# Kernel optimization log

Hardware: AMD Instinct MI355X
Metric: run time of the kernel (lower is better)

## Reference

```python
import jax, jax.numpy as jnp
import numpy as np
from itertools import permutations

EPS = 1e-14


def setup_inputs() -> dict:
    key = jax.random.key(0)
    k1, k2 = jax.random.split(key)
    B, T, S = 512, 8000, 3
    pred = jax.random.normal(k1, (B, T, S), dtype=jnp.float32)
    targets = (jax.random.uniform(k2, (B, T, S)) < 0.3).astype(jnp.float32)
    mask = jnp.ones((B, T), dtype=jnp.float32)
    return {"pred_frames_out": pred, "targets": targets, "mask": mask}


def _pit_loss(pred, targets, mask):
    # pred, targets: [B, T, S]; mask: [B, T]
    B, T, S = pred.shape
    x = pred[:, :, :, None]        # [B,T,S_pred,1]
    t = targets[:, :, None, :]     # [B,T,1,S_tgt]
    # numerically stable BCE-with-logits (same as nn.BCEWithLogitsLoss)
    bce = jnp.maximum(x, 0.0) - x * t + jnp.log1p(jnp.exp(-jnp.abs(x)))  # [B,T,S,S]
    msum = jnp.sum(mask, axis=1) + EPS                                    # [B]
    # cost[b,i,j] = masked mean over time of BCE(pred_i, target_j)
    cost = jnp.einsum('btij,bt->bij', bce, mask) / msum[:, None, None]    # [B,S,S]
    perms = jnp.asarray(list(permutations(range(S))), dtype=jnp.int32)    # [P,S]
    idx_i = jnp.arange(S)[None, :]                                        # [1,S]
    # perm_loss[b,p] = mean_i cost[b, i, perms[p,i]]
    perm_loss = jnp.mean(cost[:, idx_i, perms], axis=-1)                  # [B,P]
    best_val = jnp.min(perm_loss, axis=1)                                 # [B]
    best_idx = jnp.argmin(perm_loss, axis=1)                              # [B]
    return best_val.mean(), best_idx


def reference(pred_frames_out, targets, mask):
    return _pit_loss(pred_frames_out, targets, mask)
```

## Files before the change

kernel.cpp:

```cpp
#include <hip/hip_runtime.h>
#include <math.h>

#define BB 512
#define TT 8000
#define CH 4
#define TC (TT/CH)
#define NACC 13

__device__ __forceinline__ void accum_elem(float acc[NACC], float m,
                                           float x0, float x1, float x2,
                                           float t0, float t1, float t2) {
    acc[12] += m;
    float x[3] = {x0, x1, x2};
    float t[3] = {t0, t1, t2};
    #pragma unroll
    for (int i = 0; i < 3; i++) {
        float xi = x[i];
        float sp = fmaxf(xi, 0.0f) + __logf(1.0f + __expf(-fabsf(xi)));
        acc[i] = fmaf(m, sp, acc[i]);
        float mx = m * xi;
        #pragma unroll
        for (int j = 0; j < 3; j++)
            acc[3 + i*3 + j] = fmaf(mx, t[j], acc[3 + i*3 + j]);
    }
}

__global__ __launch_bounds__(256) void pit_partial(
        const float* __restrict__ pred,
        const float* __restrict__ tgt,
        const float* __restrict__ mask,
        float* __restrict__ bpart) {
    __shared__ float red[4][16];

    int blk = blockIdx.x;
    int b = blk >> 2, c = blk & 3;
    const float* pp = pred + ((size_t)b * TT + c * TC) * 3;
    const float* tp = tgt  + ((size_t)b * TT + c * TC) * 3;
    const float* mp = mask + (size_t)b * TT + c * TC;

    int tid = threadIdx.x;
    float acc[NACC];
    #pragma unroll
    for (int k = 0; k < NACC; k++) acc[k] = 0.0f;

    #pragma unroll
    for (int it = 0; it < 8; it++) {
        int t = tid + it * 256;
        int tc_ = t < TC ? t : TC - 1;
        float3 x3 = *(const float3*)(pp + 3 * (size_t)tc_);
        float3 g3 = *(const float3*)(tp + 3 * (size_t)tc_);
        float m = mp[tc_];
        m = (t < TC) ? m : 0.0f;
        accum_elem(acc, m, x3.x, x3.y, x3.z, g3.x, g3.y, g3.z);
    }

    #pragma unroll
    for (int k = 0; k < NACC; k++) {
        float v = acc[k];
        #pragma unroll
        for (int o = 32; o > 0; o >>= 1) v += __shfl_xor(v, o, 64);
        acc[k] = v;
    }

    int lane = tid & 63, w = tid >> 6;
    if (lane == 0) {
        #pragma unroll
        for (int k = 0; k < NACC; k++) red[w][k] = acc[k];
        red[w][13] = 0.0f; red[w][14] = 0.0f; red[w][15] = 0.0f;
    }
    __syncthreads();
    if (tid < 16) {
        float s = red[0][tid] + red[1][tid] + red[2][tid] + red[3][tid];
        bpart[(size_t)blk * 16 + tid] = s;
    }
}

__global__ __launch_bounds__(512) void pit_final(
        const float* __restrict__ bpart, float* __restrict__ out) {
    __shared__ double sd[8];
    int b = threadIdx.x;

    double a[NACC];
    #pragma unroll
    for (int k = 0; k < NACC; k++) a[k] = 0.0;
    const float* r = bpart + (size_t)b * 64;
    #pragma unroll
    for (int c = 0; c < CH; c++)
        #pragma unroll
        for (int k = 0; k < NACC; k++)
            a[k] += (double)r[c * 16 + k];

    double msum = a[12] + 1e-14;
    double cost[3][3];
    #pragma unroll
    for (int i = 0; i < 3; i++)
        #pragma unroll
        for (int j = 0; j < 3; j++)
            cost[i][j] = (a[i] - a[3 + i*3 + j]) / msum;

    const int perms[6][3] = {{0,1,2},{0,2,1},{1,0,2},{1,2,0},{2,0,1},{2,1,0}};
    double best = 1e300; int bidx = 0;
    #pragma unroll
    for (int p = 0; p < 6; p++) {
        double v = (cost[0][perms[p][0]] + cost[1][perms[p][1]] +
                    cost[2][perms[p][2]]) / 3.0;
        if (v < best) { best = v; bidx = p; }
    }
    out[1 + b] = (float)bidx;

    double v = best;
    #pragma unroll
    for (int o = 32; o > 0; o >>= 1) v += __shfl_down(v, o, 64);
    int lane = b & 63, w = b >> 6;
    if (lane == 0) sd[w] = v;
    __syncthreads();
    if (b == 0) {
        double s = 0.0;
        #pragma unroll
        for (int i = 0; i < 8; i++) s += sd[i];
        out[0] = (float)(s / (double)BB);
    }
}

extern "C" void kernel_launch(void* const* d_in, const int* in_sizes, int n_in,
                              void* d_out, int out_size, void* d_ws, size_t ws_size,
                              hipStream_t stream) {
    const float* pred = (const float*)d_in[0];
    const float* tgt  = (const float*)d_in[1];
    const float* mask = (const float*)d_in[2];
    float* out = (float*)d_out;
    float* bpart = (float*)d_ws;

    pit_partial<<<BB * CH, 256, 0, stream>>>(pred, tgt, mask, bpart);
    pit_final<<<1, 512, 0, stream>>>(bpart, out);
}
```

Measured before the change: 30.30 us.

## Use one 1024-thread block per batch and compute the permutation cost in-block

Replaces 4 blocks of 256 threads per batch with a single 1024-thread block per batch. The cost matrix and best permutation are now computed inside each block, so the final kernel only averages 512 doubles. This moves the per-batch double-precision work out of the serial single-block kernel and shrinks the workspace. The trade-offs are fewer, larger blocks (512), which may hurt occupancy and load balance across CUs, and a serial 16-way shared-memory sum done by one thread.

```diff
diff --git a/kernel.cpp b/kernel.cpp
--- a/kernel.cpp
+++ b/kernel.cpp
@@ -3,9 +3,8 @@
 
 #define BB 512
 #define TT 8000
-#define CH 4
-#define TC (TT/CH)
 #define NACC 13
+#define NW 16
 
 __device__ __forceinline__ void accum_elem(float acc[NACC], float m,
                                            float x0, float x1, float x2,
@@ -25,18 +24,18 @@
     }
 }
 
-__global__ __launch_bounds__(256) void pit_partial(
+__global__ __launch_bounds__(1024) void pit_batch(
         const float* __restrict__ pred,
         const float* __restrict__ tgt,
         const float* __restrict__ mask,
-        float* __restrict__ bpart) {
-    __shared__ float red[4][16];
+        double* __restrict__ bestv,
+        float* __restrict__ out) {
+    __shared__ float red[NW][16];
 
-    int blk = blockIdx.x;
-    int b = blk >> 2, c = blk & 3;
-    const float* pp = pred + ((size_t)b * TT + c * TC) * 3;
-    const float* tp = tgt  + ((size_t)b * TT + c * TC) * 3;
-    const float* mp = mask + (size_t)b * TT + c * TC;
+    int b = blockIdx.x;
+    const float* pp = pred + (size_t)b * TT * 3;
+    const float* tp = tgt  + (size_t)b * TT * 3;
+    const float* mp = mask + (size_t)b * TT;
 
     int tid = threadIdx.x;
     float acc[NACC];
@@ -45,12 +44,12 @@
 
     #pragma unroll
     for (int it = 0; it < 8; it++) {
-        int t = tid + it * 256;
-        int tc_ = t < TC ? t : TC - 1;
+        int t = tid + it * 1024;
+        int tc_ = t < TT ? t : TT - 1;
         float3 x3 = *(const float3*)(pp + 3 * (size_t)tc_);
         float3 g3 = *(const float3*)(tp + 3 * (size_t)tc_);
         float m = mp[tc_];
-        m = (t < TC) ? m : 0.0f;
+        m = (t < TT) ? m : 0.0f;
         accum_elem(acc, m, x3.x, x3.y, x3.z, g3.x, g3.y, g3.z);
     }
 
@@ -66,49 +65,45 @@
     if (lane == 0) {
         #pragma unroll
         for (int k = 0; k < NACC; k++) red[w][k] = acc[k];
-        red[w][13] = 0.0f; red[w][14] = 0.0f; red[w][15] = 0.0f;
     }
     __syncthreads();
-    if (tid < 16) {
-        float s = red[0][tid] + red[1][tid] + red[2][tid] + red[3][tid];
-        bpart[(size_t)blk * 16 + tid] = s;
+
+    if (tid == 0) {
+        double a[NACC];
+        #pragma unroll
+        for (int k = 0; k < NACC; k++) {
+            double s = 0.0;
+            #pragma unroll
+            for (int i = 0; i < NW; i++) s += (double)red[i][k];
+            a[k] = s;
+        }
+        double msum = a[12] + 1e-14;
+        double cost[3][3];
+        #pragma unroll
+        for (int i = 0; i < 3; i++)
+            #pragma unroll
+            for (int j = 0; j < 3; j++)
+                cost[i][j] = (a[i] - a[3 + i*3 + j]) / msum;
+
+        const int perms[6][3] = {{0,1,2},{0,2,1},{1,0,2},
+                                 {1,2,0},{2,0,1},{2,1,0}};
+        double best = 1e300; int bidx = 0;
+        #pragma unroll
+        for (int p = 0; p < 6; p++) {
+            double v = (cost[0][perms[p][0]] + cost[1][perms[p][1]] +
+                        cost[2][perms[p][2]]) / 3.0;
+            if (v < best) { best = v; bidx = p; }
+        }
+        bestv[b] = best;
+        out[1 + b] = (float)bidx;
     }
 }
 
-__global__ __launch_bounds__(512) void pit_final(
-        const float* __restrict__ bpart, float* __restrict__ out) {
+__global__ __launch_bounds__(512) void pit_mean(
+        const double* __restrict__ bestv, float* __restrict__ out) {
     __shared__ double sd[8];
     int b = threadIdx.x;
-
-    double a[NACC];
-    #pragma unroll
-    for (int k = 0; k < NACC; k++) a[k] = 0.0;
-    const float* r = bpart + (size_t)b * 64;
-    #pragma unroll
-    for (int c = 0; c < CH; c++)
-        #pragma unroll
-        for (int k = 0; k < NACC; k++)
-            a[k] += (double)r[c * 16 + k];
-
-    double msum = a[12] + 1e-14;
-    double cost[3][3];
-    #pragma unroll
-    for (int i = 0; i < 3; i++)
-        #pragma unroll
-        for (int j = 0; j < 3; j++)
-            cost[i][j] = (a[i] - a[3 + i*3 + j]) / msum;
-
-    const int perms[6][3] = {{0,1,2},{0,2,1},{1,0,2},{1,2,0},{2,0,1},{2,1,0}};
-    double best = 1e300; int bidx = 0;
-    #pragma unroll
-    for (int p = 0; p < 6; p++) {
-        double v = (cost[0][perms[p][0]] + cost[1][perms[p][1]] +
-                    cost[2][perms[p][2]]) / 3.0;
-        if (v < best) { best = v; bidx = p; }
-    }
-    out[1 + b] = (float)bidx;
-
-    double v = best;
+    double v = bestv[b];
     #pragma unroll
     for (int o = 32; o > 0; o >>= 1) v += __shfl_down(v, o, 64);
     int lane = b & 63, w = b >> 6;
@@ -129,8 +124,8 @@
     const float* tgt  = (const float*)d_in[1];
     const float* mask = (const float*)d_in[2];
     float* out = (float*)d_out;
-    float* bpart = (float*)d_ws;
+    double* bestv = (double*)d_ws;
 
-    pit_partial<<<BB * CH, 256, 0, stream>>>(pred, tgt, mask, bpart);
-    pit_final<<<1, 512, 0, stream>>>(bpart, out);
+    pit_batch<<<BB, 1024, 0, stream>>>(pred, tgt, mask, bestv, out);
+    pit_mean<<<1, 512, 0, stream>>>(bestv, out);
 }
```

Result: slower. 35.24 us (+16.3%).

## Halve block count per batch and batch loads four-deep per thread

Applied to the files above, without the earlier changes.

Each batch row is now split into two chunks of 4000 frames instead of four chunks of 2000, so 1024 blocks each process 16 frames per thread. Loads are grouped four at a time before the compute step, which exposes more memory-level parallelism per thread. The final kernel sums two partials per batch instead of four. This trades fewer blocks and less partial-sum traffic for longer per-thread loops and fewer waves available to hide latency on the device.

```diff
diff --git a/kernel.cpp b/kernel.cpp
--- a/kernel.cpp
+++ b/kernel.cpp
@@ -3,8 +3,7 @@
 
 #define BB 512
 #define TT 8000
-#define CH 4
-#define TC (TT/CH)
+#define HALF 4000
 #define NACC 13
 
 __device__ __forceinline__ void accum_elem(float acc[NACC], float m,
@@ -33,10 +32,11 @@
     __shared__ float red[4][16];
 
     int blk = blockIdx.x;
-    int b = blk >> 2, c = blk & 3;
-    const float* pp = pred + ((size_t)b * TT + c * TC) * 3;
-    const float* tp = tgt  + ((size_t)b * TT + c * TC) * 3;
-    const float* mp = mask + (size_t)b * TT + c * TC;
+    int b = blk >> 1, h = blk & 1;
+    int base = h * HALF;
+    const float* pp = pred + (size_t)b * TT * 3;
+    const float* tp = tgt  + (size_t)b * TT * 3;
+    const float* mp = mask + (size_t)b * TT;
 
     int tid = threadIdx.x;
     float acc[NACC];
@@ -44,14 +44,22 @@
     for (int k = 0; k < NACC; k++) acc[k] = 0.0f;
 
     #pragma unroll
-    for (int it = 0; it < 8; it++) {
-        int t = tid + it * 256;
-        int tc_ = t < TC ? t : TC - 1;
-        float3 x3 = *(const float3*)(pp + 3 * (size_t)tc_);
-        float3 g3 = *(const float3*)(tp + 3 * (size_t)tc_);
-        float m = mp[tc_];
-        m = (t < TC) ? m : 0.0f;
-        accum_elem(acc, m, x3.x, x3.y, x3.z, g3.x, g3.y, g3.z);
+    for (int g = 0; g < 4; g++) {
+        float3 X[4], G[4]; float M[4];
+        #pragma unroll
+        for (int u = 0; u < 4; u++) {
+            int t = base + tid + (g * 4 + u) * 256;
+            int hi = base + HALF;
+            int tc_ = t < hi ? t : hi - 1;
+            X[u] = *(const float3*)(pp + 3 * (size_t)tc_);
+            G[u] = *(const float3*)(tp + 3 * (size_t)tc_);
+            float m = mp[tc_];
+            M[u] = (t < hi) ? m : 0.0f;
+        }
+        #pragma unroll
+        for (int u = 0; u < 4; u++)
+            accum_elem(acc, M[u], X[u].x, X[u].y, X[u].z,
+                       G[u].x, G[u].y, G[u].z);
     }
 
     #pragma unroll
@@ -81,14 +89,10 @@
     int b = threadIdx.x;
 
     double a[NACC];
+    const float* r = bpart + (size_t)b * 32;
     #pragma unroll
-    for (int k = 0; k < NACC; k++) a[k] = 0.0;
-    const float* r = bpart + (size_t)b * 64;
-    #pragma unroll
-    for (int c = 0; c < CH; c++)
-        #pragma unroll
-        for (int k = 0; k < NACC; k++)
-            a[k] += (double)r[c * 16 + k];
+    for (int k = 0; k < NACC; k++)
+        a[k] = (double)r[k] + (double)r[16 + k];
 
     double msum = a[12] + 1e-14;
     double cost[3][3];
@@ -131,6 +135,6 @@
     float* out = (float*)d_out;
     float* bpart = (float*)d_ws;
 
-    pit_partial<<<BB * CH, 256, 0, stream>>>(pred, tgt, mask, bpart);
+    pit_partial<<<BB * 2, 256, 0, stream>>>(pred, tgt, mask, bpart);
     pit_final<<<1, 512, 0, stream>>>(bpart, out);
 }
```

Result: faster. 27.87 us (median of 2 runs) (-8.0%).
